# Optimization experiments

Hardware: AMD Instinct MI355X
Metric: run time of the kernel (lower is better)

Reference implementation:

```python
import jax, jax.numpy as jnp
import numpy as np

N, B, FD, D, MSG, SCN, H, FFN = 2048, 16, 128, 32, 32, 16, 4, 64
HD = D // H


def _lin(k, o, i, scale=0.05):
    kw, kb = jax.random.split(k)
    return (jax.random.normal(kw, (o, i), jnp.float32) * scale,
            jax.random.normal(kb, (o,), jnp.float32) * scale)


def setup_inputs() -> dict:
    key = jax.random.key(0)
    ks = jax.random.split(key, 24)
    inp = {}
    inp['src'] = jax.random.randint(ks[0], (B,), 0, N)
    inp['dst'] = jax.random.randint(ks[1], (B,), 0, N)
    inp['edge_feat'] = jax.random.normal(ks[2], (B, 3), jnp.float32)
    inp['timestamps'] = jax.random.uniform(ks[3], (B,), dtype=jnp.float32)
    inp['node_features'] = jax.random.normal(ks[4], (N, FD), jnp.float32)
    inp['adj'] = jnp.zeros((N, N), jnp.float32)  # unused: assume_identity_adj=True
    inp['memory'] = jax.random.normal(ks[5], (N, D), jnp.float32) * 0.1
    inp['W_emb'], inp['b_emb'] = _lin(ks[6], D, FD)
    inp['Wqkv'], inp['bqkv'] = _lin(ks[7], 3 * D, D)
    inp['Wo'], inp['bo'] = _lin(ks[8], D, D)
    inp['g1'] = jnp.ones((D,), jnp.float32); inp['be1'] = jnp.zeros((D,), jnp.float32)
    inp['g2'] = jnp.ones((D,), jnp.float32); inp['be2'] = jnp.zeros((D,), jnp.float32)
    inp['W_f1'], inp['b_f1'] = _lin(ks[9], FFN, D)
    inp['W_f2'], inp['b_f2'] = _lin(ks[10], D, FFN)
    inp['W_scn'], inp['b_scn'] = _lin(ks[11], SCN, D)
    inp['g_scn'] = jnp.ones((SCN,), jnp.float32); inp['be_scn'] = jnp.zeros((SCN,), jnp.float32)
    inp['W_e1'], inp['b_e1'] = _lin(ks[12], 32, 2 * SCN)
    inp['W_e2'], inp['b_e2'] = _lin(ks[13], 16, 32)
    inp['W_e3'], inp['b_e3'] = _lin(ks[14], 1, 16)
    inp['gru_Wih'], inp['gru_bih'] = _lin(ks[15], 3 * D, MSG)
    inp['gru_Whh'], inp['gru_bhh'] = _lin(ks[16], 3 * D, D)
    inp['W_m1'], inp['b_m1'] = _lin(ks[17], MSG, 2 * D + 3)
    inp['W_m2'], inp['b_m2'] = _lin(ks[18], MSG, MSG)
    return inp


def _ln(x, g, b):
    mu = x.mean(-1, keepdims=True)
    var = ((x - mu) ** 2).mean(-1, keepdims=True)
    return (x - mu) * jax.lax.rsqrt(var + 1e-5) * g + b


def _gru(x, h, Wih, Whh, bih, bhh):
    # torch.nn.GRUCell semantics
    gi = x @ Wih.T + bih
    gh = h @ Whh.T + bhh
    ir, iz, i_n = jnp.split(gi, 3, -1)
    hr, hz, h_n = jnp.split(gh, 3, -1)
    r = jax.nn.sigmoid(ir + hr)
    z = jax.nn.sigmoid(iz + hz)
    n = jnp.tanh(i_n + r * h_n)
    return (1.0 - z) * n + z * h


def _update_memory(memory, src, dst, edge_feat,
                   gru_Wih, gru_Whh, gru_bih, gru_bhh, W_m1, b_m1, W_m2, b_m2):
    # messages computed from pre-update memory (as in torch source)
    msg_in = jnp.concatenate([memory[src], memory[dst], edge_feat], axis=1)  # [B, 2D+3]
    messages = jax.nn.relu(msg_in @ W_m1.T + b_m1) @ W_m2.T + b_m2           # [B, MSG]

    def step(mem, inp):
        s, d, m = inp
        hs = _gru(m, mem[s], gru_Wih, gru_Whh, gru_bih, gru_bhh)
        mem = mem.at[s].set(hs)
        hd = _gru(m, mem[d], gru_Wih, gru_Whh, gru_bih, gru_bhh)  # sees updated mem if d==s earlier
        mem = mem.at[d].set(hd)
        return mem, None

    new_mem, _ = jax.lax.scan(step, memory, (src, dst, messages))
    return new_mem


def _edge_logits(node_features, src, dst,
                 W_emb, b_emb, Wqkv, bqkv, Wo, bo, g1, be1, g2, be2,
                 W_f1, b_f1, W_f2, b_f2, W_scn, b_scn, g_scn, be_scn,
                 W_e1, b_e1, W_e2, b_e2, W_e3, b_e3):
    x0 = node_features @ W_emb.T + b_emb                      # [N, D]
    x = jnp.broadcast_to(x0[None], (B, N, D))                 # [B, N, D]
    # --- Graph transformer layer (MHA, eval mode: dropout = identity) ---
    qkv = x @ Wqkv.T + bqkv                                   # [B, N, 3D]
    q, k, v = jnp.split(qkv, 3, -1)
    q = q.reshape(B, N, H, HD)
    k = k.reshape(B, N, H, HD)
    v = v.reshape(B, N, H, HD)
    scores = jnp.einsum('bqhd,bkhd->bhqk', q, k) / np.sqrt(HD)
    attn = jax.nn.softmax(scores, axis=-1)
    ao = jnp.einsum('bhqk,bkhd->bqhd', attn, v).reshape(B, N, D)
    ao = ao @ Wo.T + bo
    x = _ln(x + ao, g1, be1)
    ffn = jax.nn.gelu(x @ W_f1.T + b_f1, approximate=False) @ W_f2.T + b_f2
    x = _ln(x + ffn, g2, be2)
    # --- SCN layer (identity adjacency assumed) ---
    s_out = jax.nn.relu(_ln(x @ W_scn.T + b_scn, g_scn, be_scn))  # [B, N, SCN]
    bi = jnp.arange(B)
    src_emb = s_out[bi, src]
    dst_emb = s_out[bi, dst]
    h = jnp.concatenate([src_emb, dst_emb], axis=-1)
    h = jax.nn.relu(h @ W_e1.T + b_e1)
    h = jax.nn.relu(h @ W_e2.T + b_e2)
    return (h @ W_e3.T + b_e3).squeeze(-1)                    # [B]


def reference(src, dst, edge_feat, timestamps, node_features, adj, memory,
              W_emb, b_emb, Wqkv, bqkv, Wo, bo, g1, be1, g2, be2,
              W_f1, b_f1, W_f2, b_f2, W_scn, b_scn, g_scn, be_scn,
              W_e1, b_e1, W_e2, b_e2, W_e3, b_e3,
              gru_Wih, gru_bih, gru_Whh, gru_bhh, W_m1, b_m1, W_m2, b_m2):
    new_mem = _update_memory(memory, src, dst, edge_feat,
                             gru_Wih, gru_Whh, gru_bih, gru_bhh,
                             W_m1, b_m1, W_m2, b_m2)
    edge_logit = _edge_logits(node_features, src, dst,
                              W_emb, b_emb, Wqkv, bqkv, Wo, bo, g1, be1, g2, be2,
                              W_f1, b_f1, W_f2, b_f2, W_scn, b_scn, g_scn, be_scn,
                              W_e1, b_e1, W_e2, b_e2, W_e3, b_e3)
    return edge_logit, new_mem
```

## Files before the change

kernel.cpp:

```cpp
#include <hip/hip_runtime.h>
#include <math.h>

#define NN   2048
#define BB   16

#define WS_X0   0
#define WS_QT   65536
#define WS_KT   131072
#define WS_VT   196608
#define WS_PART 262144
#define WS_GI   268800

__device__ __forceinline__ float sigmoidf_(float x) { return 1.0f / (1.0f + __expf(-x)); }
__device__ __forceinline__ float tanhf_(float x) {
    float ex = __expf(2.0f * x);
    return 1.0f - 2.0f / (ex + 1.0f);
}
__device__ __forceinline__ float dot4_(float4 a, float4 b) {
    return a.x*b.x + a.y*b.y + a.z*b.z + a.w*b.w;
}

__global__ __launch_bounds__(256) void k1_embed_qkv(
    const float* __restrict__ nf, const float* __restrict__ Wemb, const float* __restrict__ bemb,
    const float* __restrict__ Wqkv, const float* __restrict__ bqkv,
    const float* __restrict__ mem, const int* __restrict__ src, const int* __restrict__ dst,
    const float* __restrict__ ef,
    const float* __restrict__ Wm1, const float* __restrict__ bm1,
    const float* __restrict__ Wm2, const float* __restrict__ bm2,
    const float* __restrict__ Wih, const float* __restrict__ bih,
    float* __restrict__ ws, float* __restrict__ out)
{
    __shared__ float We_s[32 * 130];
    __shared__ float nf_s[8 * 130];
    __shared__ float x0_s[8 * 33];
    __shared__ float Wq_s[96 * 33];
    __shared__ __align__(16) float Wm1_s[32 * 67];
    __shared__ float Wm2_s[32 * 33];
    __shared__ float Wih_s[96 * 33];
    __shared__ float min_s[16 * 67];
    __shared__ float mr_s[16 * 33];
    __shared__ float msg_s[16 * 33];

    const int t = threadIdx.x, bx = blockIdx.x;

    if (bx == 256) {
        float4 rm1[3], rm2, rih[3];
        float rmin[5];
        #pragma unroll
        for (int k = 0; k < 3; ++k) {
            int idx = t + 256 * k;
            rm1[k] = (idx < 536) ? ((const float4*)Wm1)[idx] : make_float4(0,0,0,0);
        }
        rm2 = ((const float4*)Wm2)[t];
        #pragma unroll
        for (int k = 0; k < 3; ++k) rih[k] = ((const float4*)Wih)[t + 256 * k];
        #pragma unroll
        for (int k = 0; k < 5; ++k) {
            int idx = t + 256 * k;
            rmin[k] = 0.f;
            if (idx < 1072) {
                int e = idx / 67, i = idx - e * 67;
                if (i < 32)      rmin[k] = mem[src[e] * 32 + i];
                else if (i < 64) rmin[k] = mem[dst[e] * 32 + (i - 32)];
                else             rmin[k] = ef[e * 3 + (i - 64)];
            }
        }
        #pragma unroll
        for (int k = 0; k < 3; ++k) {
            int idx = t + 256 * k;
            if (idx < 536) ((float4*)Wm1_s)[idx] = rm1[k];
        }
        { int o = t >> 3, i = (t & 7) * 4;
          Wm2_s[o * 33 + i] = rm2.x; Wm2_s[o * 33 + i + 1] = rm2.y;
          Wm2_s[o * 33 + i + 2] = rm2.z; Wm2_s[o * 33 + i + 3] = rm2.w; }
        #pragma unroll
        for (int k = 0; k < 3; ++k) {
            int idx = t + 256 * k;
            int o = idx >> 3, i = (idx & 7) * 4;
            Wih_s[o * 33 + i] = rih[k].x; Wih_s[o * 33 + i + 1] = rih[k].y;
            Wih_s[o * 33 + i + 2] = rih[k].z; Wih_s[o * 33 + i + 3] = rih[k].w;
        }
        #pragma unroll
        for (int k = 0; k < 5; ++k) {
            int idx = t + 256 * k;
            if (idx < 1072) min_s[idx] = rmin[k];
        }
        __syncthreads();
        {
            int o = t & 31, e0 = t >> 5;
            for (int p = 0; p < 2; ++p) {
                int e = e0 + p * 8;
                float acc = bm1[o];
                for (int i = 0; i < 67; ++i) acc += Wm1_s[o * 67 + i] * min_s[e * 67 + i];
                mr_s[e * 33 + o] = fmaxf(acc, 0.f);
            }
        }
        __syncthreads();
        {
            int o = t & 31, e0 = t >> 5;
            for (int p = 0; p < 2; ++p) {
                int e = e0 + p * 8;
                float acc = bm2[o];
                #pragma unroll 8
                for (int i = 0; i < 32; ++i) acc += Wm2_s[o * 33 + i] * mr_s[e * 33 + i];
                msg_s[e * 33 + o] = acc;
            }
        }
        __syncthreads();
        {
            float* gi_g = ws + WS_GI;
            for (int idx = t; idx < 1536; idx += 256) {
                int e = idx / 96, o = idx - e * 96;
                float acc = bih[o];
                #pragma unroll 8
                for (int i = 0; i < 32; ++i) acc += Wih_s[o * 33 + i] * msg_s[e * 33 + i];
                gi_g[idx] = acc;
            }
        }
        return;
    }

    float4 rA[4], rB[3], rC;
    #pragma unroll
    for (int k = 0; k < 4; ++k) rA[k] = ((const float4*)Wemb)[t + 256 * k];
    #pragma unroll
    for (int k = 0; k < 3; ++k) rB[k] = ((const float4*)Wqkv)[t + 256 * k];
    rC = ((const float4*)nf)[bx * 256 + t];

    if (bx < 64) {
        int g = bx * 256 + t;
        ((float4*)(out + 16))[g] = ((const float4*)mem)[g];
    }

    #pragma unroll
    for (int k = 0; k < 4; ++k) {
        int idx = t + 256 * k;
        int r = idx >> 5, c = (idx & 31) * 4;
        We_s[r * 130 + c] = rA[k].x; We_s[r * 130 + c + 1] = rA[k].y;
        We_s[r * 130 + c + 2] = rA[k].z; We_s[r * 130 + c + 3] = rA[k].w;
    }
    #pragma unroll
    for (int k = 0; k < 3; ++k) {
        int idx = t + 256 * k;
        int r = idx >> 3, c = (idx & 7) * 4;
        Wq_s[r * 33 + c] = rB[k].x; Wq_s[r * 33 + c + 1] = rB[k].y;
        Wq_s[r * 33 + c + 2] = rB[k].z; Wq_s[r * 33 + c + 3] = rB[k].w;
    }
    {
        int r = t >> 5, c = (t & 31) * 4;
        nf_s[r * 130 + c] = rC.x; nf_s[r * 130 + c + 1] = rC.y;
        nf_s[r * 130 + c + 2] = rC.z; nf_s[r * 130 + c + 3] = rC.w;
    }
    __syncthreads();

    const int j = t >> 5, o = t & 31;
    const int n = bx * 8 + j;

    float acc = bemb[o];
    {
        const float2* Wr = (const float2*)&We_s[o * 130];
        const float2* Nr = (const float2*)&nf_s[j * 130];
        float sx = 0.f, sy = 0.f;
        #pragma unroll 16
        for (int i = 0; i < 64; ++i) {
            float2 w = Wr[i], x = Nr[i];
            sx += w.x * x.x; sy += w.y * x.y;
        }
        acc += sx + sy;
    }
    x0_s[j * 33 + o] = acc;
    ws[WS_X0 + n * 32 + o] = acc;
    __syncthreads();

    #pragma unroll
    for (int c = 0; c < 3; ++c) {
        int oo = c * 32 + o;
        float a2 = bqkv[oo];
        #pragma unroll 8
        for (int i = 0; i < 32; ++i) a2 += Wq_s[oo * 33 + i] * x0_s[j * 33 + i];
        int h = o >> 3, d = o & 7;
        float* base = ws + (c == 0 ? WS_QT : (c == 1 ? WS_KT : WS_VT));
        base[h * 16384 + n * 8 + d] = a2;
    }
}

__global__ __launch_bounds__(256) void k2_attn(
    const int* __restrict__ src, const int* __restrict__ dst,
    float* __restrict__ ws)
{
    const int t = threadIdx.x, bx = blockIdx.x;
    const int s  = bx >> 2;
    const int ks = bx & 3;
    const int h  = t >> 6;
    const int l  = t & 63;

    const int e = s >> 1;
    const int n = (s & 1) ? dst[e] : src[e];

    const float* qg = ws + WS_QT + h * 16384 + n * 8;
    const float4 qa  = *(const float4*)qg;
    const float4 qb4 = *(const float4*)(qg + 4);
    const float* kbase = ws + WS_KT + h * 16384;
    const float* vbase = ws + WS_VT + h * 16384;

    float4 oa = make_float4(0.f, 0.f, 0.f, 0.f);
    float4 ob = make_float4(0.f, 0.f, 0.f, 0.f);
    float ssum = 0.f;
    const float scale = 0.35355339059327373f;

    #pragma unroll
    for (int i = 0; i < 8; ++i) {
        const int key = ks * 512 + i * 64 + l;
        const float4 ka = *(const float4*)(kbase + key * 8);
        const float4 kb = *(const float4*)(kbase + key * 8 + 4);
        const float sc = (dot4_(qa, ka) + dot4_(qb4, kb)) * scale;
        const float p = __expf(sc);
        ssum += p;
        const float4 va = *(const float4*)(vbase + key * 8);
        const float4 vb = *(const float4*)(vbase + key * 8 + 4);
        oa.x += p * va.x; oa.y += p * va.y; oa.z += p * va.z; oa.w += p * va.w;
        ob.x += p * vb.x; ob.y += p * vb.y; ob.z += p * vb.z; ob.w += p * vb.w;
    }

    #pragma unroll
    for (int m = 1; m <= 32; m <<= 1) {
        ssum += __shfl_xor(ssum, m);
        oa.x += __shfl_xor(oa.x, m); oa.y += __shfl_xor(oa.y, m);
        oa.z += __shfl_xor(oa.z, m); oa.w += __shfl_xor(oa.w, m);
        ob.x += __shfl_xor(ob.x, m); ob.y += __shfl_xor(ob.y, m);
        ob.z += __shfl_xor(ob.z, m); ob.w += __shfl_xor(ob.w, m);
    }
    if (l == 0) {
        float* p = ws + WS_PART + ((s * 4 + h) * 4 + ks) * 12;
        *(float4*)p       = oa;
        *(float4*)(p + 4) = ob;
        p[8] = ssum;
    }
}

__global__ __launch_bounds__(256, 1) void k34_post_scan(
    const int* __restrict__ src, const int* __restrict__ dst,
    const float* __restrict__ mem,
    const float* __restrict__ Wo, const float* __restrict__ bo,
    const float* __restrict__ g1, const float* __restrict__ be1,
    const float* __restrict__ Wf1, const float* __restrict__ bf1,
    const float* __restrict__ Wf2, const float* __restrict__ bf2,
    const float* __restrict__ g2, const float* __restrict__ be2,
    const float* __restrict__ Wscn, const float* __restrict__ bscn,
    const float* __restrict__ gscn, const float* __restrict__ bescn,
    const float* __restrict__ Whh, const float* __restrict__ bhh,
    const float* __restrict__ We1, const float* __restrict__ be1e,
    const float* __restrict__ We2, const float* __restrict__ be2e,
    const float* __restrict__ We3, const float* __restrict__ be3,
    float* __restrict__ ws, float* __restrict__ out)
{
    __shared__ float Wo_s[32 * 33];
    __shared__ float Wf1_s[64 * 33];
    __shared__ float Wf2_s[32 * 65];
    __shared__ float Ws_s[16 * 33];
    __shared__ float arow[32 * 33];
    __shared__ float x1s[32 * 33];
    __shared__ float fs[32 * 65];
    __shared__ float sout_s[32 * 17];
    __shared__ float We1_s[32 * 33];
    __shared__ float We2_s[16 * 33];
    __shared__ float gi_s[16 * 97];
    __shared__ __align__(16) float slots[32 * 36];
    __shared__ int nid_s[32], fid_s[32], last_s[32];

    const int t = threadIdx.x;
    const int j0 = t >> 5, o = t & 31;

    float4 w1[8], w2[8], w3[8];
    float b1 = 0.f, b2 = 0.f, b3 = 0.f;
    if (t < 64) {
        const int r2 = (t < 32) ? t + 64 : t - 32;
        const int r3 = t + 32;
        #pragma unroll
        for (int c = 0; c < 8; ++c) {
            w1[c] = ((const float4*)Whh)[t * 8 + c];
            w2[c] = ((const float4*)Whh)[r2 * 8 + c];
            w3[c] = ((const float4*)Whh)[r3 * 8 + c];
        }
        b1 = bhh[t]; b2 = bhh[r2]; b3 = bhh[r3];
    }

    float4 rWo, rF1a, rF1b, rF2a, rF2b, rE1, rWs, rE2, rG0, rG1;
    rWo  = ((const float4*)Wo)[t];
    rF1a = ((const float4*)Wf1)[t]; rF1b = ((const float4*)Wf1)[t + 256];
    rF2a = ((const float4*)Wf2)[t]; rF2b = ((const float4*)Wf2)[t + 256];
    rE1  = ((const float4*)We1)[t];
    rG0  = ((const float4*)(ws + WS_GI))[t];
    if (t < 128) {
        rWs = ((const float4*)Wscn)[t];
        rE2 = ((const float4*)We2)[t];
        rG1 = ((const float4*)(ws + WS_GI))[t + 256];
    }
    if (t < 32) nid_s[t] = (t & 1) ? dst[t >> 1] : src[t >> 1];

    { int r = t >> 3, c = (t & 7) * 4;
      Wo_s[r * 33 + c] = rWo.x; Wo_s[r * 33 + c + 1] = rWo.y;
      Wo_s[r * 33 + c + 2] = rWo.z; Wo_s[r * 33 + c + 3] = rWo.w;
      We1_s[r * 33 + c] = rE1.x; We1_s[r * 33 + c + 1] = rE1.y;
      We1_s[r * 33 + c + 2] = rE1.z; We1_s[r * 33 + c + 3] = rE1.w; }
    { int r = t >> 3, c = (t & 7) * 4;
      Wf1_s[r * 33 + c] = rF1a.x; Wf1_s[r * 33 + c + 1] = rF1a.y;
      Wf1_s[r * 33 + c + 2] = rF1a.z; Wf1_s[r * 33 + c + 3] = rF1a.w;
      int r2 = (t + 256) >> 3, c2 = ((t + 256) & 7) * 4;
      Wf1_s[r2 * 33 + c2] = rF1b.x; Wf1_s[r2 * 33 + c2 + 1] = rF1b.y;
      Wf1_s[r2 * 33 + c2 + 2] = rF1b.z; Wf1_s[r2 * 33 + c2 + 3] = rF1b.w; }
    { int r = t >> 4, c = (t & 15) * 4;
      Wf2_s[r * 65 + c] = rF2a.x; Wf2_s[r * 65 + c + 1] = rF2a.y;
      Wf2_s[r * 65 + c + 2] = rF2a.z; Wf2_s[r * 65 + c + 3] = rF2a.w;
      int r2 = (t + 256) >> 4, c2 = ((t + 256) & 15) * 4;
      Wf2_s[r2 * 65 + c2] = rF2b.x; Wf2_s[r2 * 65 + c2 + 1] = rF2b.y;
      Wf2_s[r2 * 65 + c2 + 2] = rF2b.z; Wf2_s[r2 * 65 + c2 + 3] = rF2b.w; }
    { int f = 4 * t, e = f / 96, off = f - e * 96;
      gi_s[e * 97 + off] = rG0.x; gi_s[e * 97 + off + 1] = rG0.y;
      gi_s[e * 97 + off + 2] = rG0.z; gi_s[e * 97 + off + 3] = rG0.w; }
    if (t < 128) {
        int r = t >> 3, c = (t & 7) * 4;
        Ws_s[r * 33 + c] = rWs.x; Ws_s[r * 33 + c + 1] = rWs.y;
        Ws_s[r * 33 + c + 2] = rWs.z; Ws_s[r * 33 + c + 3] = rWs.w;
        We2_s[r * 33 + c] = rE2.x; We2_s[r * 33 + c + 1] = rE2.y;
        We2_s[r * 33 + c + 2] = rE2.z; We2_s[r * 33 + c + 3] = rE2.w;
        int f = 4 * (t + 256), e2 = f / 96, off = f - e2 * 96;
        gi_s[e2 * 97 + off] = rG1.x; gi_s[e2 * 97 + off + 1] = rG1.y;
        gi_s[e2 * 97 + off + 2] = rG1.z; gi_s[e2 * 97 + off + 3] = rG1.w;
    }

    float x0v[4];
    #pragma unroll
    for (int si = 0; si < 4; ++si) {
        const int jj = si * 8 + j0;
        const int ej = jj >> 1;
        const int n = (jj & 1) ? dst[ej] : src[ej];
        const int h = o >> 3, d = o & 7;
        float num = 0.f, den = 0.f;
        #pragma unroll
        for (int ks = 0; ks < 4; ++ks) {
            const float* p = ws + WS_PART + ((jj * 4 + h) * 4 + ks) * 12;
            num += p[d];
            den += p[8];
        }
        arow[jj * 33 + o] = num / den;
        x0v[si] = ws[WS_X0 + n * 32 + o];
    }
    __syncthreads();

    if (t < 32) {
        int me = nid_s[t], f = t;
        for (int j2 = 0; j2 < t; ++j2) if (nid_s[j2] == me) { f = j2; break; }
        fid_s[t] = f;
        int isl = 1;
        for (int j2 = t + 1; j2 < 32; ++j2) if (nid_s[j2] == me) { isl = 0; break; }
        last_s[t] = isl;
    }
    __syncthreads();

    #pragma unroll
    for (int k = 0; k < 4; ++k) {
        int j2 = j0 + 8 * k;
        if (fid_s[j2] == j2) slots[j2 * 36 + o] = mem[nid_s[j2] * 32 + o];
    }

    #pragma unroll
    for (int si = 0; si < 4; ++si) {
        const int jj = si * 8 + j0;
        float a = bo[o];
        #pragma unroll 8
        for (int i = 0; i < 32; ++i) a += Wo_s[o * 33 + i] * arow[jj * 33 + i];
        float t1 = x0v[si] + a;
        float mu = t1;
        #pragma unroll
        for (int m = 16; m >= 1; m >>= 1) mu += __shfl_xor(mu, m, 32);
        mu *= (1.f / 32.f);
        float dv = t1 - mu;
        float var = dv * dv;
        #pragma unroll
        for (int m = 16; m >= 1; m >>= 1) var += __shfl_xor(var, m, 32);
        var *= (1.f / 32.f);
        x1s[jj * 33 + o] = dv * rsqrtf(var + 1e-5f) * g1[o] + be1[o];
    }
    __syncthreads();

    #pragma unroll
    for (int si = 0; si < 4; ++si) {
        const int jj = si * 8 + j0;
        #pragma unroll
        for (int c = 0; c < 2; ++c) {
            int oo = c * 32 + o;
            float f = bf1[oo];
            #pragma unroll 8
            for (int i = 0; i < 32; ++i) f += Wf1_s[oo * 33 + i] * x1s[jj * 33 + i];
            fs[jj * 65 + oo] = 0.5f * f * (1.f + erff(f * 0.70710678118654752f));
        }
    }
    __syncthreads();

    #pragma unroll
    for (int si = 0; si < 4; ++si) {
        const int jj = si * 8 + j0;
        float f2 = bf2[o];
        #pragma unroll 8
        for (int i = 0; i < 64; ++i) f2 += Wf2_s[o * 65 + i] * fs[jj * 65 + i];
        float t2 = x1s[jj * 33 + o] + f2;
        float mu2 = t2;
        #pragma unroll
        for (int m = 16; m >= 1; m >>= 1) mu2 += __shfl_xor(mu2, m, 32);
        mu2 *= (1.f / 32.f);
        float dv2 = t2 - mu2;
        float var2 = dv2 * dv2;
        #pragma unroll
        for (int m = 16; m >= 1; m >>= 1) var2 += __shfl_xor(var2, m, 32);
        var2 *= (1.f / 32.f);
        x1s[jj * 33 + o] = dv2 * rsqrtf(var2 + 1e-5f) * g2[o] + be2[o];
    }
    __syncthreads();

    if (o < 16) {
        #pragma unroll
        for (int si = 0; si < 4; ++si) {
            const int jj = si * 8 + j0;
            float sc = bscn[o];
            #pragma unroll 8
            for (int i = 0; i < 32; ++i) sc += Ws_s[o * 33 + i] * x1s[jj * 33 + i];
            float m16 = sc;
            #pragma unroll
            for (int m = 8; m >= 1; m >>= 1) m16 += __shfl_xor(m16, m, 16);
            m16 *= (1.f / 16.f);
            float d16 = sc - m16;
            float v16 = d16 * d16;
            #pragma unroll
            for (int m = 8; m >= 1; m >>= 1) v16 += __shfl_xor(v16, m, 16);
            v16 *= (1.f / 16.f);
            float sv = d16 * rsqrtf(v16 + 1e-5f) * gscn[o] + bescn[o];
            sout_s[jj * 17 + o] = fmaxf(sv, 0.f);
        }
    }
    __syncthreads();

    #pragma unroll
    for (int k = 0; k < 2; ++k) {
        int idx = t + 256 * k;
        int e = idx >> 5, i = idx & 31;
        arow[e * 33 + i] = (i < 16) ? sout_s[(2 * e) * 17 + i]
                                    : sout_s[(2 * e + 1) * 17 + (i - 16)];
    }
    __syncthreads();

    #pragma unroll
    for (int k = 0; k < 2; ++k) {
        int e = j0 + 8 * k;
        float acc = be1e[o];
        #pragma unroll 8
        for (int i = 0; i < 32; ++i) acc += We1_s[o * 33 + i] * arow[e * 33 + i];
        fs[e * 33 + o] = fmaxf(acc, 0.f);
    }
    __syncthreads();

    {
        int e = t >> 4, o2 = t & 15;
        float acc = be2e[o2];
        #pragma unroll 8
        for (int i = 0; i < 32; ++i) acc += We2_s[o2 * 33 + i] * fs[e * 33 + i];
        fs[600 + e * 17 + o2] = fmaxf(acc, 0.f);
    }
    __syncthreads();

    if (t < 16) {
        float acc = be3[0];
        #pragma unroll
        for (int i = 0; i < 16; ++i) acc += We3[i] * fs[600 + t * 17 + i];
        out[t] = acc;
    }
    __syncthreads();

    if (t < 64) {
        const bool lowhalf = (t < 32);
        for (int e = 0; e < 16; ++e) {
            const int js = 2 * e, jd = 2 * e + 1;
            const int ss = fid_s[js], sd = fid_s[jd];
            const bool same = (nid_s[js] == nid_s[jd]);
            const int npass = same ? 2 : 1;
            for (int pass = 0; pass < npass; ++pass) {
                const bool do_src = (!same) || (pass == 0);
                const bool do_dst = (!same) || (pass == 1);
                float acc1 = b1, acc2 = b2, acc3 = b3;
                #pragma unroll
                for (int c = 0; c < 8; ++c) {
                    const float4 hs4 = *(const float4*)&slots[ss * 36 + 4 * c];
                    const float4 hd4 = *(const float4*)&slots[sd * 36 + 4 * c];
                    acc1 += dot4_(w1[c], hs4);
                    const float4 hm = lowhalf ? hs4 : hd4;
                    acc2 += dot4_(w2[c], hm);
                    acc3 += dot4_(w3[c], hd4);
                }
                const float shv = __shfl_xor(lowhalf ? acc3 : acc1, 32);
                const float hr = lowhalf ? acc1 : acc2;
                const float hz = shv;
                const float hn = lowhalf ? acc2 : acc3;
                const float ir  = gi_s[e * 97 + o];
                const float iz  = gi_s[e * 97 + 32 + o];
                const float inn = gi_s[e * 97 + 64 + o];
                const float r = sigmoidf_(ir + hr);
                const float z = sigmoidf_(iz + hz);
                const float nn = tanhf_(inn + r * hn);
                const int slot = lowhalf ? ss : sd;
                const float hold = slots[slot * 36 + o];
                const float hnew = (1.f - z) * nn + z * hold;
                const bool wr = lowhalf ? do_src : do_dst;
                if (wr) slots[slot * 36 + o] = hnew;
                __threadfence_block();
            }
        }
    }
    __syncthreads();

    #pragma unroll
    for (int k = 0; k < 4; ++k) {
        int j2 = j0 + 8 * k;
        if (last_s[j2]) out[16 + nid_s[j2] * 32 + o] = slots[fid_s[j2] * 36 + o];
    }
}

extern "C" void kernel_launch(void* const* d_in, const int* in_sizes, int n_in,
                              void* d_out, int out_size, void* d_ws, size_t ws_size,
                              hipStream_t stream)
{
    (void)in_sizes; (void)n_in; (void)out_size; (void)ws_size;
    const int*   src   = (const int*)d_in[0];
    const int*   dst   = (const int*)d_in[1];
    const float* ef    = (const float*)d_in[2];
    const float* nf    = (const float*)d_in[4];
    const float* mem   = (const float*)d_in[6];
    const float* Wemb  = (const float*)d_in[7];
    const float* bemb  = (const float*)d_in[8];
    const float* Wqkv  = (const float*)d_in[9];
    const float* bqkv  = (const float*)d_in[10];
    const float* Wo    = (const float*)d_in[11];
    const float* bo    = (const float*)d_in[12];
    const float* g1    = (const float*)d_in[13];
    const float* be1   = (const float*)d_in[14];
    const float* g2    = (const float*)d_in[15];
    const float* be2   = (const float*)d_in[16];
    const float* Wf1   = (const float*)d_in[17];
    const float* bf1   = (const float*)d_in[18];
    const float* Wf2   = (const float*)d_in[19];
    const float* bf2   = (const float*)d_in[20];
    const float* Wscn  = (const float*)d_in[21];
    const float* bscn  = (const float*)d_in[22];
    const float* gscn  = (const float*)d_in[23];
    const float* bescn = (const float*)d_in[24];
    const float* We1   = (const float*)d_in[25];
    const float* be1e  = (const float*)d_in[26];
    const float* We2   = (const float*)d_in[27];
    const float* be2e  = (const float*)d_in[28];
    const float* We3   = (const float*)d_in[29];
    const float* be3   = (const float*)d_in[30];
    const float* Wih   = (const float*)d_in[31];
    const float* bih   = (const float*)d_in[32];
    const float* Whh   = (const float*)d_in[33];
    const float* bhh   = (const float*)d_in[34];
    const float* Wm1   = (const float*)d_in[35];
    const float* bm1   = (const float*)d_in[36];
    const float* Wm2   = (const float*)d_in[37];
    const float* bm2   = (const float*)d_in[38];
    float* out = (float*)d_out;
    float* ws  = (float*)d_ws;

    hipLaunchKernelGGL(k1_embed_qkv, dim3(257), dim3(256), 0, stream,
        nf, Wemb, bemb, Wqkv, bqkv, mem, src, dst, ef, Wm1, bm1, Wm2, bm2, Wih, bih, ws, out);
    hipLaunchKernelGGL(k2_attn, dim3(128), dim3(256), 0, stream, src, dst, ws);
    hipLaunchKernelGGL(k34_post_scan, dim3(1), dim3(256), 0, stream,
        src, dst, mem, Wo, bo, g1, be1, Wf1, bf1, Wf2, bf2, g2, be2,
        Wscn, bscn, gscn, bescn, Whh, bhh, We1, be1e, We2, be2e, We3, be3, ws, out);
}
```

Baseline: 179.5 us.

## Merge attention into post-scan kernel with flag sync; spread message MLP across blocks

Drops the separate attention launch. Attention partial sums now run in all 128 blocks of the post-scan kernel, and block 0 spins on global flags until every block has published its partials, then runs the serial tail. The per-edge message MLP and GRU input projection move out of a dedicated extra block and are spread over the first 16 embedding blocks, one edge each, so the 257th block no longer sits on the critical path. This saves a launch gap and the serial 16-edge MLP, but adds a spin-wait that relies on all blocks being co-resident, plus flag resets in the first kernel.

```diff
diff --git a/kernel.cpp b/kernel.cpp
--- a/kernel.cpp
+++ b/kernel.cpp
@@ -10,6 +10,7 @@
 #define WS_VT   196608
 #define WS_PART 262144
 #define WS_GI   268800
+#define WS_FLAG 270336
 
 __device__ __forceinline__ float sigmoidf_(float x) { return 1.0f / (1.0f + __expf(-x)); }
 __device__ __forceinline__ float tanhf_(float x) {
@@ -20,7 +21,7 @@
     return a.x*b.x + a.y*b.y + a.z*b.z + a.w*b.w;
 }
 
-__global__ __launch_bounds__(256) void k1_embed_qkv(
+__global__ __launch_bounds__(256) void kA_embed_qkv_msg(
     const float* __restrict__ nf, const float* __restrict__ Wemb, const float* __restrict__ bemb,
     const float* __restrict__ Wqkv, const float* __restrict__ bqkv,
     const float* __restrict__ mem, const int* __restrict__ src, const int* __restrict__ dst,
@@ -34,101 +35,45 @@
     __shared__ float nf_s[8 * 130];
     __shared__ float x0_s[8 * 33];
     __shared__ float Wq_s[96 * 33];
-    __shared__ __align__(16) float Wm1_s[32 * 67];
+    __shared__ __align__(16) float Wm1_s[2144];
     __shared__ float Wm2_s[32 * 33];
     __shared__ float Wih_s[96 * 33];
-    __shared__ float min_s[16 * 67];
-    __shared__ float mr_s[16 * 33];
-    __shared__ float msg_s[16 * 33];
+    __shared__ float min_s[67];
+    __shared__ float mr_s[32];
+    __shared__ float msg_s[32];
 
     const int t = threadIdx.x, bx = blockIdx.x;
-
-    if (bx == 256) {
-        float4 rm1[3], rm2, rih[3];
-        float rmin[5];
+    const bool domsg = (bx < 16);
+
+    float4 rA[4], rB[3], rC;
+    #pragma unroll
+    for (int k = 0; k < 4; ++k) rA[k] = ((const float4*)Wemb)[t + 256 * k];
+    #pragma unroll
+    for (int k = 0; k < 3; ++k) rB[k] = ((const float4*)Wqkv)[t + 256 * k];
+    rC = ((const float4*)nf)[bx * 256 + t];
+
+    float4 rm1[3], rm2v, rih[3];
+    float rminv = 0.f;
+    if (domsg) {
         #pragma unroll
         for (int k = 0; k < 3; ++k) {
             int idx = t + 256 * k;
             rm1[k] = (idx < 536) ? ((const float4*)Wm1)[idx] : make_float4(0,0,0,0);
         }
-        rm2 = ((const float4*)Wm2)[t];
+        rm2v = ((const float4*)Wm2)[t];
         #pragma unroll
         for (int k = 0; k < 3; ++k) rih[k] = ((const float4*)Wih)[t + 256 * k];
-        #pragma unroll
-        for (int k = 0; k < 5; ++k) {
-            int idx = t + 256 * k;
-            rmin[k] = 0.f;
-            if (idx < 1072) {
-                int e = idx / 67, i = idx - e * 67;
-                if (i < 32)      rmin[k] = mem[src[e] * 32 + i];
-                else if (i < 64) rmin[k] = mem[dst[e] * 32 + (i - 32)];
-                else             rmin[k] = ef[e * 3 + (i - 64)];
-            }
-        }
-        #pragma unroll
-        for (int k = 0; k < 3; ++k) {
-            int idx = t + 256 * k;
-            if (idx < 536) ((float4*)Wm1_s)[idx] = rm1[k];
-        }
-        { int o = t >> 3, i = (t & 7) * 4;
-          Wm2_s[o * 33 + i] = rm2.x; Wm2_s[o * 33 + i + 1] = rm2.y;
-          Wm2_s[o * 33 + i + 2] = rm2.z; Wm2_s[o * 33 + i + 3] = rm2.w; }
-        #pragma unroll
-        for (int k = 0; k < 3; ++k) {
-            int idx = t + 256 * k;
-            int o = idx >> 3, i = (idx & 7) * 4;
-            Wih_s[o * 33 + i] = rih[k].x; Wih_s[o * 33 + i + 1] = rih[k].y;
-            Wih_s[o * 33 + i + 2] = rih[k].z; Wih_s[o * 33 + i + 3] = rih[k].w;
-        }
-        #pragma unroll
-        for (int k = 0; k < 5; ++k) {
-            int idx = t + 256 * k;
-            if (idx < 1072) min_s[idx] = rmin[k];
-        }
-        __syncthreads();
-        {
-            int o = t & 31, e0 = t >> 5;
-            for (int p = 0; p < 2; ++p) {
-                int e = e0 + p * 8;
-                float acc = bm1[o];
-                for (int i = 0; i < 67; ++i) acc += Wm1_s[o * 67 + i] * min_s[e * 67 + i];
-                mr_s[e * 33 + o] = fmaxf(acc, 0.f);
-            }
-        }
-        __syncthreads();
-        {
-            int o = t & 31, e0 = t >> 5;
-            for (int p = 0; p < 2; ++p) {
-                int e = e0 + p * 8;
-                float acc = bm2[o];
-                #pragma unroll 8
-                for (int i = 0; i < 32; ++i) acc += Wm2_s[o * 33 + i] * mr_s[e * 33 + i];
-                msg_s[e * 33 + o] = acc;
-            }
-        }
-        __syncthreads();
-        {
-            float* gi_g = ws + WS_GI;
-            for (int idx = t; idx < 1536; idx += 256) {
-                int e = idx / 96, o = idx - e * 96;
-                float acc = bih[o];
-                #pragma unroll 8
-                for (int i = 0; i < 32; ++i) acc += Wih_s[o * 33 + i] * msg_s[e * 33 + i];
-                gi_g[idx] = acc;
-            }
-        }
-        return;
-    }
-
-    float4 rA[4], rB[3], rC;
-    #pragma unroll
-    for (int k = 0; k < 4; ++k) rA[k] = ((const float4*)Wemb)[t + 256 * k];
-    #pragma unroll
-    for (int k = 0; k < 3; ++k) rB[k] = ((const float4*)Wqkv)[t + 256 * k];
-    rC = ((const float4*)nf)[bx * 256 + t];
-
-    if (bx < 64) {
-        int g = bx * 256 + t;
+        if (t < 67) {
+            const int e = bx;
+            rminv = (t < 32) ? mem[src[e] * 32 + t]
+                  : (t < 64) ? mem[dst[e] * 32 + (t - 32)]
+                             : ef[e * 3 + (t - 64)];
+        }
+    }
+
+    if (bx == 255 && t < 128) ((unsigned*)(ws + WS_FLAG))[t] = 0u;
+    if (bx >= 16 && bx < 80) {
+        int g = (bx - 16) * 256 + t;
         ((float4*)(out + 16))[g] = ((const float4*)mem)[g];
     }
 
@@ -150,6 +95,24 @@
         int r = t >> 5, c = (t & 31) * 4;
         nf_s[r * 130 + c] = rC.x; nf_s[r * 130 + c + 1] = rC.y;
         nf_s[r * 130 + c + 2] = rC.z; nf_s[r * 130 + c + 3] = rC.w;
+    }
+    if (domsg) {
+        #pragma unroll
+        for (int k = 0; k < 3; ++k) {
+            int idx = t + 256 * k;
+            if (idx < 536) ((float4*)Wm1_s)[idx] = rm1[k];
+        }
+        { int r = t >> 3, c = (t & 7) * 4;
+          Wm2_s[r * 33 + c] = rm2v.x; Wm2_s[r * 33 + c + 1] = rm2v.y;
+          Wm2_s[r * 33 + c + 2] = rm2v.z; Wm2_s[r * 33 + c + 3] = rm2v.w; }
+        #pragma unroll
+        for (int k = 0; k < 3; ++k) {
+            int idx = t + 256 * k;
+            int r = idx >> 3, c = (idx & 7) * 4;
+            Wih_s[r * 33 + c] = rih[k].x; Wih_s[r * 33 + c + 1] = rih[k].y;
+            Wih_s[r * 33 + c + 2] = rih[k].z; Wih_s[r * 33 + c + 3] = rih[k].w;
+        }
+        if (t < 67) min_s[t] = rminv;
     }
     __syncthreads();
 
@@ -170,6 +133,11 @@
     }
     x0_s[j * 33 + o] = acc;
     ws[WS_X0 + n * 32 + o] = acc;
+    if (domsg && t < 32) {
+        float a1 = bm1[t];
+        for (int i = 0; i < 67; ++i) a1 += Wm1_s[t * 67 + i] * min_s[i];
+        mr_s[t] = fmaxf(a1, 0.f);
+    }
     __syncthreads();
 
     #pragma unroll
@@ -182,63 +150,23 @@
         float* base = ws + (c == 0 ? WS_QT : (c == 1 ? WS_KT : WS_VT));
         base[h * 16384 + n * 8 + d] = a2;
     }
+    if (domsg && t < 32) {
+        float a2 = bm2[t];
+        #pragma unroll 8
+        for (int i = 0; i < 32; ++i) a2 += Wm2_s[t * 33 + i] * mr_s[i];
+        msg_s[t] = a2;
+    }
+    __syncthreads();
+
+    if (domsg && t < 96) {
+        float a3 = bih[t];
+        #pragma unroll 8
+        for (int i = 0; i < 32; ++i) a3 += Wih_s[t * 33 + i] * msg_s[i];
+        ws[WS_GI + bx * 96 + t] = a3;
+    }
 }
 
-__global__ __launch_bounds__(256) void k2_attn(
-    const int* __restrict__ src, const int* __restrict__ dst,
-    float* __restrict__ ws)
-{
-    const int t = threadIdx.x, bx = blockIdx.x;
-    const int s  = bx >> 2;
-    const int ks = bx & 3;
-    const int h  = t >> 6;
-    const int l  = t & 63;
-
-    const int e = s >> 1;
-    const int n = (s & 1) ? dst[e] : src[e];
-
-    const float* qg = ws + WS_QT + h * 16384 + n * 8;
-    const float4 qa  = *(const float4*)qg;
-    const float4 qb4 = *(const float4*)(qg + 4);
-    const float* kbase = ws + WS_KT + h * 16384;
-    const float* vbase = ws + WS_VT + h * 16384;
-
-    float4 oa = make_float4(0.f, 0.f, 0.f, 0.f);
-    float4 ob = make_float4(0.f, 0.f, 0.f, 0.f);
-    float ssum = 0.f;
-    const float scale = 0.35355339059327373f;
-
-    #pragma unroll
-    for (int i = 0; i < 8; ++i) {
-        const int key = ks * 512 + i * 64 + l;
-        const float4 ka = *(const float4*)(kbase + key * 8);
-        const float4 kb = *(const float4*)(kbase + key * 8 + 4);
-        const float sc = (dot4_(qa, ka) + dot4_(qb4, kb)) * scale;
-        const float p = __expf(sc);
-        ssum += p;
-        const float4 va = *(const float4*)(vbase + key * 8);
-        const float4 vb = *(const float4*)(vbase + key * 8 + 4);
-        oa.x += p * va.x; oa.y += p * va.y; oa.z += p * va.z; oa.w += p * va.w;
-        ob.x += p * vb.x; ob.y += p * vb.y; ob.z += p * vb.z; ob.w += p * vb.w;
-    }
-
-    #pragma unroll
-    for (int m = 1; m <= 32; m <<= 1) {
-        ssum += __shfl_xor(ssum, m);
-        oa.x += __shfl_xor(oa.x, m); oa.y += __shfl_xor(oa.y, m);
-        oa.z += __shfl_xor(oa.z, m); oa.w += __shfl_xor(oa.w, m);
-        ob.x += __shfl_xor(ob.x, m); ob.y += __shfl_xor(ob.y, m);
-        ob.z += __shfl_xor(ob.z, m); ob.w += __shfl_xor(ob.w, m);
-    }
-    if (l == 0) {
-        float* p = ws + WS_PART + ((s * 4 + h) * 4 + ks) * 12;
-        *(float4*)p       = oa;
-        *(float4*)(p + 4) = ob;
-        p[8] = ssum;
-    }
-}
-
-__global__ __launch_bounds__(256, 1) void k34_post_scan(
+__global__ __launch_bounds__(256, 1) void kB_attn_post_scan(
     const int* __restrict__ src, const int* __restrict__ dst,
     const float* __restrict__ mem,
     const float* __restrict__ Wo, const float* __restrict__ bo,
@@ -268,42 +196,101 @@
     __shared__ __align__(16) float slots[32 * 36];
     __shared__ int nid_s[32], fid_s[32], last_s[32];
 
-    const int t = threadIdx.x;
-    const int j0 = t >> 5, o = t & 31;
+    const int t = threadIdx.x, bx = blockIdx.x;
+    unsigned* flags = (unsigned*)(ws + WS_FLAG);
 
     float4 w1[8], w2[8], w3[8];
     float b1 = 0.f, b2 = 0.f, b3 = 0.f;
-    if (t < 64) {
-        const int r2 = (t < 32) ? t + 64 : t - 32;
-        const int r3 = t + 32;
-        #pragma unroll
-        for (int c = 0; c < 8; ++c) {
-            w1[c] = ((const float4*)Whh)[t * 8 + c];
-            w2[c] = ((const float4*)Whh)[r2 * 8 + c];
-            w3[c] = ((const float4*)Whh)[r3 * 8 + c];
-        }
-        b1 = bhh[t]; b2 = bhh[r2]; b3 = bhh[r3];
-    }
-
     float4 rWo, rF1a, rF1b, rF2a, rF2b, rE1, rWs, rE2, rG0, rG1;
-    rWo  = ((const float4*)Wo)[t];
-    rF1a = ((const float4*)Wf1)[t]; rF1b = ((const float4*)Wf1)[t + 256];
-    rF2a = ((const float4*)Wf2)[t]; rF2b = ((const float4*)Wf2)[t + 256];
-    rE1  = ((const float4*)We1)[t];
-    rG0  = ((const float4*)(ws + WS_GI))[t];
+    if (bx == 0) {
+        if (t < 64) {
+            const int r2 = (t < 32) ? t + 64 : t - 32;
+            const int r3 = t + 32;
+            #pragma unroll
+            for (int c = 0; c < 8; ++c) {
+                w1[c] = ((const float4*)Whh)[t * 8 + c];
+                w2[c] = ((const float4*)Whh)[r2 * 8 + c];
+                w3[c] = ((const float4*)Whh)[r3 * 8 + c];
+            }
+            b1 = bhh[t]; b2 = bhh[r2]; b3 = bhh[r3];
+        }
+        rWo  = ((const float4*)Wo)[t];
+        rF1a = ((const float4*)Wf1)[t]; rF1b = ((const float4*)Wf1)[t + 256];
+        rF2a = ((const float4*)Wf2)[t]; rF2b = ((const float4*)Wf2)[t + 256];
+        rE1  = ((const float4*)We1)[t];
+        rG0  = ((const float4*)(ws + WS_GI))[t];
+        if (t < 128) {
+            rWs = ((const float4*)Wscn)[t];
+            rE2 = ((const float4*)We2)[t];
+            rG1 = ((const float4*)(ws + WS_GI))[t + 256];
+        }
+        if (t < 32) nid_s[t] = (t & 1) ? dst[t >> 1] : src[t >> 1];
+    }
+
+    {
+        const int s  = bx >> 2;
+        const int ks = bx & 3;
+        const int h  = t >> 6;
+        const int l  = t & 63;
+        const int e = s >> 1;
+        const int n = (s & 1) ? dst[e] : src[e];
+
+        const float* qg = ws + WS_QT + h * 16384 + n * 8;
+        const float4 qa  = *(const float4*)qg;
+        const float4 qb4 = *(const float4*)(qg + 4);
+        const float* kbase = ws + WS_KT + h * 16384;
+        const float* vbase = ws + WS_VT + h * 16384;
+
+        float4 oa = make_float4(0.f, 0.f, 0.f, 0.f);
+        float4 ob = make_float4(0.f, 0.f, 0.f, 0.f);
+        float ssum = 0.f;
+        const float scale = 0.35355339059327373f;
+
+        #pragma unroll
+        for (int i = 0; i < 8; ++i) {
+            const int key = ks * 512 + i * 64 + l;
+            const float4 ka = *(const float4*)(kbase + key * 8);
+            const float4 kb = *(const float4*)(kbase + key * 8 + 4);
+            const float sc = (dot4_(qa, ka) + dot4_(qb4, kb)) * scale;
+            const float p = __expf(sc);
+            ssum += p;
+            const float4 va = *(const float4*)(vbase + key * 8);
+            const float4 vb = *(const float4*)(vbase + key * 8 + 4);
+            oa.x += p * va.x; oa.y += p * va.y; oa.z += p * va.z; oa.w += p * va.w;
+            ob.x += p * vb.x; ob.y += p * vb.y; ob.z += p * vb.z; ob.w += p * vb.w;
+        }
+        #pragma unroll
+        for (int m = 1; m <= 32; m <<= 1) {
+            ssum += __shfl_xor(ssum, m);
+            oa.x += __shfl_xor(oa.x, m); oa.y += __shfl_xor(oa.y, m);
+            oa.z += __shfl_xor(oa.z, m); oa.w += __shfl_xor(oa.w, m);
+            ob.x += __shfl_xor(ob.x, m); ob.y += __shfl_xor(ob.y, m);
+            ob.z += __shfl_xor(ob.z, m); ob.w += __shfl_xor(ob.w, m);
+        }
+        if (l == 0) {
+            float* p = ws + WS_PART + ((s * 4 + h) * 4 + ks) * 12;
+            *(float4*)p       = oa;
+            *(float4*)(p + 4) = ob;
+            p[8] = ssum;
+        }
+    }
+    __threadfence();
+    if (t == 0) atomicExch(&flags[bx], 1u);
+    if (bx != 0) return;
+
     if (t < 128) {
-        rWs = ((const float4*)Wscn)[t];
-        rE2 = ((const float4*)We2)[t];
-        rG1 = ((const float4*)(ws + WS_GI))[t + 256];
-    }
-    if (t < 32) nid_s[t] = (t & 1) ? dst[t >> 1] : src[t >> 1];
+        while (atomicAdd(&flags[t], 0u) == 0u) { __builtin_amdgcn_s_sleep(8); }
+    }
+    __syncthreads();
+    __threadfence();
+
+    const int j0 = t >> 5, o = t & 31;
 
     { int r = t >> 3, c = (t & 7) * 4;
       Wo_s[r * 33 + c] = rWo.x; Wo_s[r * 33 + c + 1] = rWo.y;
       Wo_s[r * 33 + c + 2] = rWo.z; Wo_s[r * 33 + c + 3] = rWo.w;
       We1_s[r * 33 + c] = rE1.x; We1_s[r * 33 + c + 1] = rE1.y;
-      We1_s[r * 33 + c + 2] = rE1.z; We1_s[r * 33 + c + 3] = rE1.w; }
-    { int r = t >> 3, c = (t & 7) * 4;
+      We1_s[r * 33 + c + 2] = rE1.z; We1_s[r * 33 + c + 3] = rE1.w;
       Wf1_s[r * 33 + c] = rF1a.x; Wf1_s[r * 33 + c + 1] = rF1a.y;
       Wf1_s[r * 33 + c + 2] = rF1a.z; Wf1_s[r * 33 + c + 3] = rF1a.w;
       int r2 = (t + 256) >> 3, c2 = ((t + 256) & 7) * 4;
@@ -569,10 +556,9 @@
     float* out = (float*)d_out;
     float* ws  = (float*)d_ws;
 
-    hipLaunchKernelGGL(k1_embed_qkv, dim3(257), dim3(256), 0, stream,
+    hipLaunchKernelGGL(kA_embed_qkv_msg, dim3(256), dim3(256), 0, stream,
         nf, Wemb, bemb, Wqkv, bqkv, mem, src, dst, ef, Wm1, bm1, Wm2, bm2, Wih, bih, ws, out);
-    hipLaunchKernelGGL(k2_attn, dim3(128), dim3(256), 0, stream, src, dst, ws);
-    hipLaunchKernelGGL(k34_post_scan, dim3(1), dim3(256), 0, stream,
+    hipLaunchKernelGGL(kB_attn_post_scan, dim3(128), dim3(256), 0, stream,
         src, dst, mem, Wo, bo, g1, be1, Wf1, bf1, Wf2, bf2, g2, be2,
         Wscn, bscn, gscn, bescn, Whh, bhh, We1, be1e, We2, be2e, We3, be3, ws, out);
 }
```

Result: slower. 184.6 us (+2.9%).
